# Performance work log

Hardware: AMD Instinct MI355X
Metric: run time of the kernel (lower is better)

## Reference

```python
import jax, jax.numpy as jnp
import numpy as np

N = 8192
E = 262144
H = 64


def setup_inputs() -> dict:
    key = jax.random.key(0)
    ks = jax.random.split(key, 9)
    edge_index = jax.random.randint(ks[0], (2, E), 0, N, dtype=jnp.int64)
    edge_attr = jax.random.uniform(ks[1], (E,), dtype=jnp.float32)
    node_features = jax.random.normal(ks[2], (N, N), dtype=jnp.float32)
    # GCNConv weights (glorot-ish scale) and biases
    W1 = jax.random.normal(ks[3], (N, H), dtype=jnp.float32) / np.sqrt(N)
    b1 = jnp.zeros((H,), dtype=jnp.float32)
    W2 = jax.random.normal(ks[4], (H, H), dtype=jnp.float32) / np.sqrt(H)
    b2 = jnp.zeros((H,), dtype=jnp.float32)
    fcW = jax.random.normal(ks[5], (H, N), dtype=jnp.float32) / np.sqrt(H)
    fcb = jnp.zeros((N,), dtype=jnp.float32)
    return {"edge_index": edge_index, "edge_attr": edge_attr,
            "node_features": node_features,
            "W1": W1, "b1": b1, "W2": W2, "b2": b2,
            "fcW": fcW, "fcb": fcb}


def _gcn_conv(x, W, b, src, dst, ew, n_nodes):
    # PyG GCNConv with edge weights: x' = D^{-1/2} (A + I) D^{-1/2} (x W) + b
    # src/dst/ew already include self-loops (weight 1.0).
    x = x @ W                                        # [N, out]
    deg = jax.ops.segment_sum(ew, dst, num_segments=n_nodes)  # in-degree w/ loops
    dinv = jax.lax.rsqrt(deg)                        # deg >= 1 due to self loops
    norm = dinv[src] * ew * dinv[dst]                # [E+N]
    out = jax.ops.segment_sum(x[src] * norm[:, None], dst, num_segments=n_nodes)
    return out + b


def reference(edge_index, edge_attr, node_features, W1, b1, W2, b2, fcW, fcb):
    n_nodes = node_features.shape[0]
    loops = jnp.arange(n_nodes, dtype=edge_index.dtype)
    src = jnp.concatenate([edge_index[0], loops])
    dst = jnp.concatenate([edge_index[1], loops])
    ew = jnp.concatenate([edge_attr, jnp.ones((n_nodes,), edge_attr.dtype)])
    x = jax.nn.relu(_gcn_conv(node_features, W1, b1, src, dst, ew, n_nodes))
    x = jax.nn.relu(_gcn_conv(x, W2, b2, src, dst, ew, n_nodes))
    x = x @ fcW + fcb
    return jax.nn.softmax(x, axis=-1)
```

## Files before the change

### kernel.cpp

```cpp
#include <hip/hip_runtime.h>


#define NN 8192
#define NE 262144
#define HD 64

typedef float f32x4 __attribute__((ext_vector_type(4)));
typedef short v8s   __attribute__((ext_vector_type(8)));
typedef unsigned short ushort_t;

__device__ __forceinline__ unsigned short bf16_rne(float f){
  union { float f; unsigned u; } v; v.f = f;
  unsigned r = v.u + 0x7fffu + ((v.u >> 16) & 1u);
  return (unsigned short)(r >> 16);
}
__device__ __forceinline__ float bf16_f32(unsigned short h){
  union { unsigned u; float f; } v; v.u = ((unsigned)h) << 16;
  return v.f;
}
__device__ __forceinline__ f32x4 mfma16(v8s a, v8s b, f32x4 c){
  return __builtin_amdgcn_mfma_f32_16x16x32_bf16(a, b, c, 0, 0, 0);
}

__global__ void k_prep0(const float* __restrict__ W1, const float* __restrict__ fcW,
                        ushort_t* w1hi, ushort_t* w1lo, ushort_t* fcwp,
                        float* deg, int* cnt, int* wcnt, float* S){
  int idx = blockIdx.x*blockDim.x + threadIdx.x;
  if (idx < NN){ deg[idx]=1.0f; cnt[idx]=0; wcnt[idx]=0; S[idx]=0.0f; }
  {
    int kk = idx & 31, c = (idx>>5)&15, nt = (idx>>9)&3, kb = idx>>11;
    int k = kb*32 + kk, col = nt*16 + c;
    float w = W1[(size_t)k*HD + col];
    unsigned short hi = bf16_rne(w);
    w1hi[idx] = hi;
    w1lo[idx] = bf16_rne(w - bf16_f32(hi));
  }
  {
    int kk = idx & 31, c = (idx>>5)&15, cblk = (idx>>9)&511, kb = idx>>18;
    int k = kb*32 + kk, col = cblk*16 + c;
    fcwp[idx] = bf16_rne(fcW[(size_t)k*NN + col]);
  }
}

__global__ void k_deg_cnt(const int* ei, const float* ew, float* deg, int* cnt){
  int e = blockIdx.x*blockDim.x + threadIdx.x;
  if (e < NE){
    int d = ei[NE + e];
    atomicAdd(&deg[d], ew[e]);
    atomicAdd(&cnt[d], 1);
  }
}

__global__ void k_scan(const int* cnt, const float* deg, int* rowptr, float* dinv){
  __shared__ int part[256];
  int t = threadIdx.x;
  int loc[32]; int s = 0;
  #pragma unroll
  for (int j=0;j<32;++j){ loc[j] = cnt[t*32+j]; s += loc[j]; }
  part[t] = s; __syncthreads();
  for (int off=1; off<256; off<<=1){
    int v = (t >= off) ? part[t-off] : 0;
    __syncthreads();
    part[t] += v;
    __syncthreads();
  }
  int run = part[t] - s;
  #pragma unroll
  for (int j=0;j<32;++j){ rowptr[t*32+j] = run; run += loc[j]; }
  if (t == 255) rowptr[NN] = run;
  #pragma unroll
  for (int j=0;j<32;++j) dinv[t*32+j] = 1.0f / sqrtf(deg[t*32+j]);
}

__global__ void k_fill(const int* ei, const float* ew, const float* dinv,
                       const int* rowptr, int* wcnt, int* csr_src, float* csr_nrm){
  int e = blockIdx.x*blockDim.x + threadIdx.x;
  if (e < NE){
    int s = ei[e], d = ei[NE+e];
    int slot = rowptr[d] + atomicAdd(&wcnt[d], 1);
    csr_src[slot] = s;
    csr_nrm[slot] = dinv[s] * ew[e] * dinv[d];
  }
}

__global__ __launch_bounds__(512) void k_gemm1(const float* __restrict__ X,
                                               const ushort_t* __restrict__ w1hi,
                                               const ushort_t* __restrict__ w1lo,
                                               float* __restrict__ xw1){
  int tid = threadIdx.x, lane = tid & 63, w = tid >> 6;
  int r = lane & 15, seg = lane >> 4;
  int row0 = blockIdx.x * 32;
  const float* xr0 = X + (size_t)(row0 + r)     * NN + seg*8;
  const float* xr1 = X + (size_t)(row0 + 16 + r)* NN + seg*8;
  int kbase = w * 1024;

  f32x4 z = {0.f,0.f,0.f,0.f};
  f32x4 acc0[4] = {z,z,z,z};
  f32x4 acc1[4] = {z,z,z,z};

  f32x4 p00 = *(const f32x4*)(xr0 + kbase);
  f32x4 p01 = *(const f32x4*)(xr0 + kbase + 4);
  f32x4 p10 = *(const f32x4*)(xr1 + kbase);
  f32x4 p11 = *(const f32x4*)(xr1 + kbase + 4);

  for (int it = 0; it < 32; ++it){
    int k0 = kbase + it*32;
    int kb = k0 >> 5;
    f32x4 c00=p00, c01=p01, c10=p10, c11=p11;
    if (it < 31){
      int kn = k0 + 32;
      p00 = *(const f32x4*)(xr0 + kn);
      p01 = *(const f32x4*)(xr0 + kn + 4);
      p10 = *(const f32x4*)(xr1 + kn);
      p11 = *(const f32x4*)(xr1 + kn + 4);
    }
    v8s a0h, a0l, a1h, a1l;
    #pragma unroll
    for (int j=0;j<4;++j){
      float f = c00[j]; unsigned short h = bf16_rne(f);
      a0h[j] = (short)h; a0l[j] = (short)bf16_rne(f - bf16_f32(h));
      f = c01[j]; h = bf16_rne(f);
      a0h[4+j] = (short)h; a0l[4+j] = (short)bf16_rne(f - bf16_f32(h));
      f = c10[j]; h = bf16_rne(f);
      a1h[j] = (short)h; a1l[j] = (short)bf16_rne(f - bf16_f32(h));
      f = c11[j]; h = bf16_rne(f);
      a1h[4+j] = (short)h; a1l[4+j] = (short)bf16_rne(f - bf16_f32(h));
    }
    #pragma unroll
    for (int nt=0; nt<4; ++nt){
      size_t boff = ((size_t)(kb*4 + nt)*16 + r)*32 + seg*8;
      v8s bh = *(const v8s*)(w1hi + boff);
      v8s bl = *(const v8s*)(w1lo + boff);
      acc0[nt] = mfma16(a0h, bh, acc0[nt]);
      acc0[nt] = mfma16(a0h, bl, acc0[nt]);
      acc0[nt] = mfma16(a0l, bh, acc0[nt]);
      acc1[nt] = mfma16(a1h, bh, acc1[nt]);
      acc1[nt] = mfma16(a1h, bl, acc1[nt]);
      acc1[nt] = mfma16(a1l, bh, acc1[nt]);
    }
  }

  __shared__ float red[8][32][65];
  #pragma unroll
  for (int nt=0; nt<4; ++nt)
    #pragma unroll
    for (int j=0;j<4;++j){
      red[w][4*seg + j][nt*16 + r]      = acc0[nt][j];
      red[w][16 + 4*seg + j][nt*16 + r] = acc1[nt][j];
    }
  __syncthreads();
  for (int o = tid; o < 32*64; o += 512){
    int rr = o >> 6, cc = o & 63;
    float s = 0.f;
    #pragma unroll
    for (int ww=0; ww<8; ++ww) s += red[ww][rr][cc];
    xw1[(size_t)(row0 + rr)*HD + cc] = s;
  }
}

__global__ __launch_bounds__(256) void k_agg1c(const float* __restrict__ xin,
                                               const float* __restrict__ b1,
                                               const float* __restrict__ W2,
                                               const float* __restrict__ dinv,
                                               const int* __restrict__ rowptr,
                                               const int* __restrict__ csr_src,
                                               const float* __restrict__ csr_nrm,
                                               float* __restrict__ x2w){
  __shared__ float W2s[64*64];
  __shared__ float rows[4][64];
  int lane = threadIdx.x & 63, w = threadIdx.x >> 6;
  for (int o = threadIdx.x; o < 64*64; o += 256) W2s[o] = W2[o];
  __syncthreads();

  int i = blockIdx.x*4 + w;
  float di = dinv[i];
  float acc = di*di * xin[(size_t)i*HD + lane];
  int e = rowptr[i], e1 = rowptr[i+1];
  for (; e + 1 < e1; e += 2){
    int s0 = csr_src[e], s1 = csr_src[e+1];
    float n0 = csr_nrm[e], n1 = csr_nrm[e+1];
    acc += n0 * xin[(size_t)s0*HD + lane];
    acc += n1 * xin[(size_t)s1*HD + lane];
  }
  if (e < e1) acc += csr_nrm[e] * xin[(size_t)csr_src[e]*HD + lane];
  float v = acc + b1[lane];
  rows[w][lane] = v > 0.f ? v : 0.f;
  __syncthreads();

  float acc2 = 0.f;
  #pragma unroll
  for (int k=0;k<64;++k) acc2 += rows[w][k] * W2s[k*64 + lane];
  x2w[(size_t)i*HD + lane] = acc2;
}

__global__ __launch_bounds__(256) void k_agg2(const float* __restrict__ xin,
                                              const float* __restrict__ b2,
                                              const float* __restrict__ dinv,
                                              const int* __restrict__ rowptr,
                                              const int* __restrict__ csr_src,
                                              const float* __restrict__ csr_nrm,
                                              ushort_t* __restrict__ x2b){
  int lane = threadIdx.x & 63, w = threadIdx.x >> 6;
  int i = blockIdx.x*4 + w;
  float di = dinv[i];
  float acc = di*di * xin[(size_t)i*HD + lane];
  int e = rowptr[i], e1 = rowptr[i+1];
  for (; e + 1 < e1; e += 2){
    int s0 = csr_src[e], s1 = csr_src[e+1];
    float n0 = csr_nrm[e], n1 = csr_nrm[e+1];
    acc += n0 * xin[(size_t)s0*HD + lane];
    acc += n1 * xin[(size_t)s1*HD + lane];
  }
  if (e < e1) acc += csr_nrm[e] * xin[(size_t)csr_src[e]*HD + lane];
  float v = acc + b2[lane];
  v = v > 0.f ? v : 0.f;
  x2b[(size_t)i*HD + lane] = bf16_rne(v);
}

__global__ __launch_bounds__(256) void k_rowsum(const ushort_t* __restrict__ x2b,
                                                const ushort_t* __restrict__ fcwp,
                                                const float* __restrict__ fcb,
                                                float* __restrict__ S){
  int lane = threadIdx.x & 63, w = threadIdx.x >> 6;
  int r = lane & 15, seg = lane >> 4;
  int row0 = blockIdx.x*128 + w*32;
  const ushort_t* xb = x2b + (size_t)(row0 + r)*HD + seg*8;
  v8s x00 = *(const v8s*)(xb);
  v8s x01 = *(const v8s*)(xb + 32);
  v8s x10 = *(const v8s*)(xb + 16*HD);
  v8s x11 = *(const v8s*)(xb + 16*HD + 32);
  float rp0 = 0.f, rp1 = 0.f;
  for (int cb=0; cb<4; ++cb){
    int colbase = blockIdx.y*256 + cb*64;
    f32x4 z = {0.f,0.f,0.f,0.f};
    f32x4 acc0[4] = {z,z,z,z}, acc1[4] = {z,z,z,z};
    #pragma unroll
    for (int nt=0; nt<4; ++nt){
      int cblk = (colbase >> 4) + nt;
      v8s bA = *(const v8s*)(fcwp + ((size_t)cblk*16 + r)*32 + seg*8);
      v8s bB = *(const v8s*)(fcwp + ((size_t)(512 + cblk)*16 + r)*32 + seg*8);
      acc0[nt] = mfma16(bA, x00, acc0[nt]);
      acc0[nt] = mfma16(bB, x01, acc0[nt]);
      acc1[nt] = mfma16(bA, x10, acc1[nt]);
      acc1[nt] = mfma16(bB, x11, acc1[nt]);
    }
    #pragma unroll
    for (int nt=0; nt<4; ++nt){
      int col = colbase + nt*16 + seg*4;
      f32x4 fb = *(const f32x4*)(fcb + col);
      #pragma unroll
      for (int j=0;j<4;++j){
        rp0 += __expf(acc0[nt][j] + fb[j]);
        rp1 += __expf(acc1[nt][j] + fb[j]);
      }
    }
  }
  rp0 += __shfl_xor(rp0, 16); rp0 += __shfl_xor(rp0, 32);
  rp1 += __shfl_xor(rp1, 16); rp1 += __shfl_xor(rp1, 32);
  if (lane < 16){
    atomicAdd(&S[row0 + lane],      rp0);
    atomicAdd(&S[row0 + 16 + lane], rp1);
  }
}

__global__ __launch_bounds__(256) void k_passB(const ushort_t* __restrict__ x2b,
                                               const ushort_t* __restrict__ fcwp,
                                               const float* __restrict__ fcb,
                                               const float* __restrict__ S,
                                               float* __restrict__ out){
  int lane = threadIdx.x & 63, w = threadIdx.x >> 6;
  int r = lane & 15, seg = lane >> 4;
  int row0 = blockIdx.x*128 + w*32;
  const ushort_t* xb = x2b + (size_t)(row0 + r)*HD + seg*8;
  v8s x00 = *(const v8s*)(xb);
  v8s x01 = *(const v8s*)(xb + 32);
  v8s x10 = *(const v8s*)(xb + 16*HD);
  v8s x11 = *(const v8s*)(xb + 16*HD + 32);
  float si0 = 1.0f / S[row0 + r];
  float si1 = 1.0f / S[row0 + 16 + r];
  float* o0 = out + (size_t)(row0 + r)*NN;
  float* o1 = out + (size_t)(row0 + 16 + r)*NN;
  for (int cb=0; cb<4; ++cb){
    int colbase = blockIdx.y*256 + cb*64;
    f32x4 z = {0.f,0.f,0.f,0.f};
    f32x4 acc0[4] = {z,z,z,z}, acc1[4] = {z,z,z,z};
    #pragma unroll
    for (int nt=0; nt<4; ++nt){
      int cblk = (colbase >> 4) + nt;
      v8s bA = *(const v8s*)(fcwp + ((size_t)cblk*16 + r)*32 + seg*8);
      v8s bB = *(const v8s*)(fcwp + ((size_t)(512 + cblk)*16 + r)*32 + seg*8);
      acc0[nt] = mfma16(bA, x00, acc0[nt]);
      acc0[nt] = mfma16(bB, x01, acc0[nt]);
      acc1[nt] = mfma16(bA, x10, acc1[nt]);
      acc1[nt] = mfma16(bB, x11, acc1[nt]);
    }
    #pragma unroll
    for (int nt=0; nt<4; ++nt){
      int col = colbase + nt*16 + seg*4;
      f32x4 fb = *(const f32x4*)(fcb + col);
      f32x4 v0, v1;
      #pragma unroll
      for (int j=0;j<4;++j){
        v0[j] = __expf(acc0[nt][j] + fb[j]) * si0;
        v1[j] = __expf(acc1[nt][j] + fb[j]) * si1;
      }
      *(f32x4*)(o0 + col) = v0;
      *(f32x4*)(o1 + col) = v1;
    }
  }
}

extern "C" void kernel_launch(void* const* d_in, const int* in_sizes, int n_in,
                              void* d_out, int out_size, void* d_ws, size_t ws_size,
                              hipStream_t stream){
  (void)in_sizes; (void)n_in; (void)out_size; (void)ws_size;
  const int*   ei  = (const int*)  d_in[0];
  const float* ew  = (const float*)d_in[1];
  const float* X   = (const float*)d_in[2];
  const float* W1  = (const float*)d_in[3];
  const float* b1  = (const float*)d_in[4];
  const float* W2  = (const float*)d_in[5];
  const float* b2  = (const float*)d_in[6];
  const float* fcW = (const float*)d_in[7];
  const float* fcb = (const float*)d_in[8];
  float* out = (float*)d_out;
  char*  ws  = (char*)d_ws;

  float*    deg     = (float*)   (ws + 0);
  float*    dinv    = (float*)   (ws + 32768);
  int*      cnt     = (int*)     (ws + 65536);
  int*      wcnt    = (int*)     (ws + 98304);
  int*      rowptr  = (int*)     (ws + 131072);
  int*      csr_src = (int*)     (ws + 167936);
  float*    csr_nrm = (float*)   (ws + 1216512);
  ushort_t* w1hi    = (ushort_t*)(ws + 2265088);
  ushort_t* w1lo    = (ushort_t*)(ws + 3313664);
  ushort_t* fcwp    = (ushort_t*)(ws + 4362240);
  float*    xw1     = (float*)   (ws + 5410816);
  float*    x2w     = (float*)   (ws + 7507968);
  ushort_t* x2b     = (ushort_t*)(ws + 9605120);
  float*    S       = (float*)   (ws + 10653696);

  k_prep0   <<<2048, 256, 0, stream>>>(W1, fcW, w1hi, w1lo, fcwp, deg, cnt, wcnt, S);
  k_deg_cnt <<<1024, 256, 0, stream>>>(ei, ew, deg, cnt);
  k_scan    <<<1,    256, 0, stream>>>(cnt, deg, rowptr, dinv);
  k_fill    <<<1024, 256, 0, stream>>>(ei, ew, dinv, rowptr, wcnt, csr_src, csr_nrm);
  k_gemm1   <<<256,  512, 0, stream>>>(X, w1hi, w1lo, xw1);
  k_agg1c   <<<2048, 256, 0, stream>>>(xw1, b1, W2, dinv, rowptr, csr_src, csr_nrm, x2w);
  k_agg2    <<<2048, 256, 0, stream>>>(x2w, b2, dinv, rowptr, csr_src, csr_nrm, x2b);
  k_rowsum  <<<dim3(64,32), 256, 0, stream>>>(x2b, fcwp, fcb, S);
  k_passB   <<<dim3(64,32), 256, 0, stream>>>(x2b, fcwp, fcb, S, out);
}
```

Baseline: 300.3 us.

## Split GEMM1 K dimension across blocks and reduce partials in separate kernel

The first GEMM changes from 256 blocks, each with 8 waves splitting K and reducing through shared memory, to a 2D grid of 128 row-blocks by 8 K-chunks. Each wave computes 16 rows over one 1024-wide K chunk and writes partial results to a global buffer. A new kernel then sums the 8 partials. The aim is more blocks in flight to saturate HBM bandwidth on the 256MB X read, at the cost of an extra launch and 16MB of partial-sum traffic.

Measured after the change: 320.8 us. 1.07x slower.

```diff
diff --git a/kernel.cpp b/kernel.cpp
--- a/kernel.cpp
+++ b/kernel.cpp
@@ -4,6 +4,8 @@
 #define NN 8192
 #define NE 262144
 #define HD 64
+#define KCH 1024
+#define NKC 8
 
 typedef float f32x4 __attribute__((ext_vector_type(4)));
 typedef short v8s   __attribute__((ext_vector_type(8)));
@@ -83,79 +85,66 @@
   }
 }
 
-__global__ __launch_bounds__(512) void k_gemm1(const float* __restrict__ X,
+__global__ __launch_bounds__(256) void k_gemm1(const float* __restrict__ X,
                                                const ushort_t* __restrict__ w1hi,
                                                const ushort_t* __restrict__ w1lo,
-                                               float* __restrict__ xw1){
-  int tid = threadIdx.x, lane = tid & 63, w = tid >> 6;
+                                               float* __restrict__ xw1p){
+  int lane = threadIdx.x & 63, w = threadIdx.x >> 6;
   int r = lane & 15, seg = lane >> 4;
-  int row0 = blockIdx.x * 32;
-  const float* xr0 = X + (size_t)(row0 + r)     * NN + seg*8;
-  const float* xr1 = X + (size_t)(row0 + 16 + r)* NN + seg*8;
-  int kbase = w * 1024;
+  int row = blockIdx.x*64 + w*16 + r;
+  int kb0 = blockIdx.y * KCH;
+  const float* xr = X + (size_t)row * NN + kb0 + seg*8;
 
   f32x4 z = {0.f,0.f,0.f,0.f};
-  f32x4 acc0[4] = {z,z,z,z};
-  f32x4 acc1[4] = {z,z,z,z};
-
-  f32x4 p00 = *(const f32x4*)(xr0 + kbase);
-  f32x4 p01 = *(const f32x4*)(xr0 + kbase + 4);
-  f32x4 p10 = *(const f32x4*)(xr1 + kbase);
-  f32x4 p11 = *(const f32x4*)(xr1 + kbase + 4);
-
-  for (int it = 0; it < 32; ++it){
-    int k0 = kbase + it*32;
-    int kb = k0 >> 5;
-    f32x4 c00=p00, c01=p01, c10=p10, c11=p11;
-    if (it < 31){
-      int kn = k0 + 32;
-      p00 = *(const f32x4*)(xr0 + kn);
-      p01 = *(const f32x4*)(xr0 + kn + 4);
-      p10 = *(const f32x4*)(xr1 + kn);
-      p11 = *(const f32x4*)(xr1 + kn + 4);
-    }
-    v8s a0h, a0l, a1h, a1l;
+  f32x4 acc[4] = {z,z,z,z};
+
+  f32x4 p0 = *(const f32x4*)(xr);
+  f32x4 p1 = *(const f32x4*)(xr + 4);
+
+  for (int it = 0; it < KCH/32; ++it){
+    f32x4 c0 = p0, c1 = p1;
+    if (it < KCH/32 - 1){
+      p0 = *(const f32x4*)(xr + (it+1)*32);
+      p1 = *(const f32x4*)(xr + (it+1)*32 + 4);
+    }
+    v8s ah, al;
     #pragma unroll
     for (int j=0;j<4;++j){
-      float f = c00[j]; unsigned short h = bf16_rne(f);
-      a0h[j] = (short)h; a0l[j] = (short)bf16_rne(f - bf16_f32(h));
-      f = c01[j]; h = bf16_rne(f);
-      a0h[4+j] = (short)h; a0l[4+j] = (short)bf16_rne(f - bf16_f32(h));
-      f = c10[j]; h = bf16_rne(f);
-      a1h[j] = (short)h; a1l[j] = (short)bf16_rne(f - bf16_f32(h));
-      f = c11[j]; h = bf16_rne(f);
-      a1h[4+j] = (short)h; a1l[4+j] = (short)bf16_rne(f - bf16_f32(h));
-    }
-    #pragma unroll
-    for (int nt=0; nt<4; ++nt){
-      size_t boff = ((size_t)(kb*4 + nt)*16 + r)*32 + seg*8;
+      float f = c0[j]; unsigned short h = bf16_rne(f);
+      ah[j] = (short)h; al[j] = (short)bf16_rne(f - bf16_f32(h));
+      f = c1[j]; h = bf16_rne(f);
+      ah[4+j] = (short)h; al[4+j] = (short)bf16_rne(f - bf16_f32(h));
+    }
+    int kbb = (kb0 >> 5) + it;
+    #pragma unroll
+    for (int nt=0; nt<4; ++nt){
+      size_t boff = ((size_t)(kbb*4 + nt)*16 + r)*32 + seg*8;
       v8s bh = *(const v8s*)(w1hi + boff);
       v8s bl = *(const v8s*)(w1lo + boff);
-      acc0[nt] = mfma16(a0h, bh, acc0[nt]);
-      acc0[nt] = mfma16(a0h, bl, acc0[nt]);
-      acc0[nt] = mfma16(a0l, bh, acc0[nt]);
-      acc1[nt] = mfma16(a1h, bh, acc1[nt]);
-      acc1[nt] = mfma16(a1h, bl, acc1[nt]);
-      acc1[nt] = mfma16(a1l, bh, acc1[nt]);
-    }
-  }
-
-  __shared__ float red[8][32][65];
+      acc[nt] = mfma16(ah, bh, acc[nt]);
+      acc[nt] = mfma16(ah, bl, acc[nt]);
+      acc[nt] = mfma16(al, bh, acc[nt]);
+    }
+  }
+
+  float* o = xw1p + (size_t)blockIdx.y*(NN*HD) + (size_t)(blockIdx.x*64 + w*16)*HD;
   #pragma unroll
   for (int nt=0; nt<4; ++nt)
     #pragma unroll
-    for (int j=0;j<4;++j){
-      red[w][4*seg + j][nt*16 + r]      = acc0[nt][j];
-      red[w][16 + 4*seg + j][nt*16 + r] = acc1[nt][j];
-    }
-  __syncthreads();
-  for (int o = tid; o < 32*64; o += 512){
-    int rr = o >> 6, cc = o & 63;
-    float s = 0.f;
-    #pragma unroll
-    for (int ww=0; ww<8; ++ww) s += red[ww][rr][cc];
-    xw1[(size_t)(row0 + rr)*HD + cc] = s;
-  }
+    for (int j=0;j<4;++j)
+      o[(4*seg + j)*HD + nt*16 + r] = acc[nt][j];
+}
+
+__global__ __launch_bounds__(256) void k_red(const float* __restrict__ xw1p,
+                                             float* __restrict__ xw1){
+  int i = blockIdx.x*blockDim.x + threadIdx.x;
+  f32x4 s = {0.f,0.f,0.f,0.f};
+  #pragma unroll
+  for (int c=0;c<NKC;++c){
+    f32x4 v = *(const f32x4*)(xw1p + (size_t)c*NN*HD + (size_t)i*4);
+    s[0]+=v[0]; s[1]+=v[1]; s[2]+=v[2]; s[3]+=v[3];
+  }
+  *(f32x4*)(xw1 + (size_t)i*4) = s;
 }
 
 __global__ __launch_bounds__(256) void k_agg1c(const float* __restrict__ xin,
@@ -336,16 +325,18 @@
   ushort_t* w1hi    = (ushort_t*)(ws + 2265088);
   ushort_t* w1lo    = (ushort_t*)(ws + 3313664);
   ushort_t* fcwp    = (ushort_t*)(ws + 4362240);
-  float*    xw1     = (float*)   (ws + 5410816);
-  float*    x2w     = (float*)   (ws + 7507968);
-  ushort_t* x2b     = (ushort_t*)(ws + 9605120);
-  float*    S       = (float*)   (ws + 10653696);
+  float*    xw1p    = (float*)   (ws + 5410816);
+  float*    xw1     = (float*)   (ws + 22188032);
+  float*    x2w     = (float*)   (ws + 24285184);
+  ushort_t* x2b     = (ushort_t*)(ws + 26382336);
+  float*    S       = (float*)   (ws + 27430912);
 
   k_prep0   <<<2048, 256, 0, stream>>>(W1, fcW, w1hi, w1lo, fcwp, deg, cnt, wcnt, S);
   k_deg_cnt <<<1024, 256, 0, stream>>>(ei, ew, deg, cnt);
   k_scan    <<<1,    256, 0, stream>>>(cnt, deg, rowptr, dinv);
   k_fill    <<<1024, 256, 0, stream>>>(ei, ew, dinv, rowptr, wcnt, csr_src, csr_nrm);
-  k_gemm1   <<<256,  512, 0, stream>>>(X, w1hi, w1lo, xw1);
+  k_gemm1   <<<dim3(128, NKC), 256, 0, stream>>>(X, w1hi, w1lo, xw1p);
+  k_red     <<<512,  256, 0, stream>>>(xw1p, xw1);
   k_agg1c   <<<2048, 256, 0, stream>>>(xw1, b1, W2, dinv, rowptr, csr_src, csr_nrm, x2w);
   k_agg2    <<<2048, 256, 0, stream>>>(x2w, b2, dinv, rowptr, csr_src, csr_nrm, x2b);
   k_rowsum  <<<dim3(64,32), 256, 0, stream>>>(x2b, fcwp, fcb, S);
```
